# Kernel optimization log

Measured on AMD Instinct MI355X. Metric: run time of the kernel, lower is better.

Reference implementation:

```python
import jax, jax.numpy as jnp
import numpy as np

BN_EPS = 1e-5

def conv1x1(x, w, b):
    # x: [B,C,H,W], w: [O,C], b: [O]
    return jnp.einsum('bchw,oc->bohw', x, w) + b[None, :, None, None]

def maxpool2x2(x):
    B, C, H, W = x.shape
    return x.reshape(B, C, H // 2, 2, W // 2, 2).max(axis=(3, 5))

def setup_inputs() -> dict:
    key = jax.random.key(0)
    ks = jax.random.split(key, 11)
    B, C, H, W = 8, 256, 64, 64
    Ci = C // 2  # inter_channels = 128
    s_in = 1.0 / np.sqrt(C)
    s_int = 1.0 / np.sqrt(Ci)
    return {
        'x': jax.random.normal(ks[0], (B, C, H, W), jnp.float32),
        'theta_w': jax.random.uniform(ks[1], (Ci, C), jnp.float32, -s_in, s_in),
        'theta_b': jax.random.uniform(ks[2], (Ci,), jnp.float32, -s_in, s_in),
        'phi_w': jax.random.uniform(ks[3], (Ci, C), jnp.float32, -s_in, s_in),
        'phi_b': jax.random.uniform(ks[4], (Ci,), jnp.float32, -s_in, s_in),
        'g_w': jax.random.uniform(ks[5], (Ci, C), jnp.float32, -s_in, s_in),
        'g_b': jax.random.uniform(ks[6], (Ci,), jnp.float32, -s_in, s_in),
        'W_w': jax.random.uniform(ks[7], (C, Ci), jnp.float32, -s_int, s_int),
        'W_b': jax.random.uniform(ks[8], (C,), jnp.float32, -s_int, s_int),
        'bn_gamma': jax.random.normal(ks[9], (C,), jnp.float32) * 0.1 + 1.0,
        'bn_beta': jax.random.normal(ks[10], (C,), jnp.float32) * 0.1,
    }

def reference(x, theta_w, theta_b, phi_w, phi_b, g_w, g_b, W_w, W_b, bn_gamma, bn_beta):
    B, C, H, W = x.shape
    Ci = theta_w.shape[0]
    # g and phi are sub-sampled (2x2 maxpool) after the 1x1 conv
    g_x = maxpool2x2(conv1x1(x, g_w, g_b)).reshape(B, Ci, -1)        # [B,Ci,M]
    g_x = g_x.transpose(0, 2, 1)                                     # [B,M,Ci]
    theta_x = conv1x1(x, theta_w, theta_b).reshape(B, Ci, -1)        # [B,Ci,N]
    theta_x = theta_x.transpose(0, 2, 1)                             # [B,N,Ci]
    phi_x = maxpool2x2(conv1x1(x, phi_w, phi_b)).reshape(B, Ci, -1)  # [B,Ci,M]
    f = jnp.einsum('bnc,bcm->bnm', theta_x, phi_x)                   # [B,N,M]
    f_div_C = jax.nn.softmax(f, axis=-1)
    y = jnp.einsum('bnm,bmc->bnc', f_div_C, g_x)                     # [B,N,Ci]
    y = y.transpose(0, 2, 1).reshape(B, Ci, H, W)
    # 1x1 conv + BatchNorm2d (training-mode batch statistics)
    W_y = conv1x1(y, W_w, W_b)
    mean = W_y.mean(axis=(0, 2, 3))
    var = W_y.var(axis=(0, 2, 3))
    W_y = (W_y - mean[None, :, None, None]) * jax.lax.rsqrt(var + BN_EPS)[None, :, None, None]
    W_y = W_y * bn_gamma[None, :, None, None] + bn_beta[None, :, None, None]
    return W_y + x
```

## Files before the change

### kernel.cpp

```cpp
#include <hip/hip_runtime.h>
#include <hip/hip_bf16.h>
#include <cstdint>
#include <math.h>

using bf16 = __hip_bfloat16;
typedef __attribute__((ext_vector_type(8))) short bf16x8;
typedef __attribute__((ext_vector_type(4))) float f32x4;

#define DEV __device__ __forceinline__

DEV float b2f(unsigned short u) { return __uint_as_float(((uint32_t)u) << 16); }
DEV float bfl(bf16 h) { return __bfloat162float(h); }
DEV short f2bs(float f) { bf16 h = __float2bfloat16(f); return *(short*)&h; }
DEV uint32_t pk2(float a, float b) {
  return (uint32_t)(unsigned short)f2bs(a) |
         ((uint32_t)(unsigned short)f2bs(b) << 16);
}
DEV float ldv(const void* p, int isbf, int i) {
  return isbf ? bfl(((const bf16*)p)[i]) : ((const float*)p)[i];
}

DEV bf16x8 load_wfrag(const void* w, int isbf, int row, int K, int off) {
  bf16x8 r;
  if (isbf) {
    r = *(const bf16x8*)((const short*)w + (size_t)row * K + off);
  } else {
    const float* f = (const float*)w + (size_t)row * K + off;
    float4 a = *(const float4*)f, b = *(const float4*)(f + 4);
    r[0] = f2bs(a.x); r[1] = f2bs(a.y); r[2] = f2bs(a.z); r[3] = f2bs(a.w);
    r[4] = f2bs(b.x); r[5] = f2bs(b.y); r[6] = f2bs(b.z); r[7] = f2bs(b.w);
  }
  return r;
}

__global__ __launch_bounds__(256) void sniff_kernel(
    const unsigned short* __restrict__ xr, int* __restrict__ flag)
{
  int tid = threadIdx.x;
  int good = 0;
  for (int k = tid; k < 16384; k += 256) {
    unsigned short u = xr[2 * k];
    int e = (u >> 7) & 0xFF;
    good += (e >= 0x6A && e <= 0x86) ? 1 : 0;
  }
  __shared__ int r[256];
  r[tid] = good;
  __syncthreads();
  for (int off = 128; off; off >>= 1) {
    if (tid < off) r[tid] += r[tid + off];
    __syncthreads();
  }
  if (tid == 0) *flag = (r[0] > 9830) ? 1 : 0;
}

__global__ __launch_bounds__(256) void transpose_x(
    const void* __restrict__ x, short* __restrict__ xT, const int* __restrict__ flag)
{
  const int isbf = *flag;
  __shared__ short lt[64 * 71];
  const int n0 = blockIdx.x * 64, c0 = blockIdx.y * 64, b = blockIdx.z;
  const int tid = threadIdx.x;
  for (int it = 0; it < 4; ++it) {
    int idx4 = it * 256 + tid;
    int ci = idx4 >> 4, n4 = (idx4 & 15) * 4;
    size_t go = ((size_t)(b * 256 + c0 + ci)) * 4096 + n0 + n4;
    if (isbf) {
      ushort4 v = *(const ushort4*)((const unsigned short*)x + go);
      lt[ci * 71 + n4 + 0] = v.x; lt[ci * 71 + n4 + 1] = v.y;
      lt[ci * 71 + n4 + 2] = v.z; lt[ci * 71 + n4 + 3] = v.w;
    } else {
      float4 v = *(const float4*)((const float*)x + go);
      lt[ci * 71 + n4 + 0] = f2bs(v.x); lt[ci * 71 + n4 + 1] = f2bs(v.y);
      lt[ci * 71 + n4 + 2] = f2bs(v.z); lt[ci * 71 + n4 + 3] = f2bs(v.w);
    }
  }
  __syncthreads();
  for (int it = 0; it < 4; ++it) {
    int idx4 = it * 256 + tid;
    int n = idx4 >> 4, c4 = (idx4 & 15) * 4;
    ushort4 v;
    v.x = (unsigned short)lt[(c4 + 0) * 71 + n];
    v.y = (unsigned short)lt[(c4 + 1) * 71 + n];
    v.z = (unsigned short)lt[(c4 + 2) * 71 + n];
    v.w = (unsigned short)lt[(c4 + 3) * 71 + n];
    *(ushort4*)(xT + ((size_t)(b * 4096 + n0 + n)) * 256 + c0 + c4) = v;
  }
}

__global__ __launch_bounds__(256) void conv_tp_k(
    const short* __restrict__ xT,
    const void* __restrict__ w1, const void* __restrict__ b1, short* __restrict__ out1,
    const void* __restrict__ w2, const void* __restrict__ b2, short* __restrict__ out2,
    const int* __restrict__ flag)
{
  const int isbf = *flag;
  __shared__ short shA[64 * 264];
  __shared__ short shB[64 * 136];
  const int b = blockIdx.y, nbase = blockIdx.x * 64, tid = threadIdx.x;
  const int ln = tid & 15, q = (tid >> 4) & 3, wv = tid >> 6;
  for (int it = 0; it < 16; ++it) {
    int idx4 = it * 256 + tid;
    int n = idx4 >> 6, c4 = (idx4 & 63) * 4;
    *(ushort4*)&shA[n * 264 + c4] =
        *(const ushort4*)(xT + ((size_t)(b * 4096 + nbase + n)) * 256 + c4);
  }
  __syncthreads();
  f32x4 zero = {0.f, 0.f, 0.f, 0.f};
  f32x4 acc1[4][2], acc2[4][2];
  for (int nt = 0; nt < 4; ++nt)
    for (int ti = 0; ti < 2; ++ti) { acc1[nt][ti] = zero; acc2[nt][ti] = zero; }

  for (int kk = 0; kk < 8; ++kk) {
    int off = kk * 32 + q * 8;
    bf16x8 a[4];
    #pragma unroll
    for (int nt = 0; nt < 4; ++nt)
      a[nt] = *(const bf16x8*)&shA[(16 * nt + ln) * 264 + off];
    #pragma unroll
    for (int ti = 0; ti < 2; ++ti) {
      bf16x8 bw1 = load_wfrag(w1, isbf, 16 * (2 * wv + ti) + ln, 256, off);
      #pragma unroll
      for (int nt = 0; nt < 4; ++nt)
        acc1[nt][ti] = __builtin_amdgcn_mfma_f32_16x16x32_bf16(a[nt], bw1, acc1[nt][ti], 0, 0, 0);
    }
    #pragma unroll
    for (int ti = 0; ti < 2; ++ti) {
      bf16x8 bw2 = load_wfrag(w2, isbf, 16 * (2 * wv + ti) + ln, 256, off);
      #pragma unroll
      for (int nt = 0; nt < 4; ++nt)
        acc2[nt][ti] = __builtin_amdgcn_mfma_f32_16x16x32_bf16(a[nt], bw2, acc2[nt][ti], 0, 0, 0);
    }
  }
  {
    float bv[2];
    for (int ti = 0; ti < 2; ++ti) bv[ti] = ldv(b1, isbf, 16 * (2 * wv + ti) + ln);
    for (int nt = 0; nt < 4; ++nt)
      for (int ti = 0; ti < 2; ++ti)
        for (int r = 0; r < 4; ++r)
          shB[(16 * nt + q * 4 + r) * 136 + 16 * (2 * wv + ti) + ln] =
              f2bs(acc1[nt][ti][r] + bv[ti]);
    __syncthreads();
    for (int it = 0; it < 8; ++it) {
      int idx4 = it * 256 + tid;
      int n = idx4 >> 5, c4 = (idx4 & 31) * 4;
      *(ushort4*)(out1 + ((size_t)(b * 4096 + nbase + n)) * 128 + c4) =
          *(const ushort4*)&shB[n * 136 + c4];
    }
    __syncthreads();
  }
  {
    float bv[2];
    for (int ti = 0; ti < 2; ++ti) bv[ti] = ldv(b2, isbf, 16 * (2 * wv + ti) + ln);
    for (int nt = 0; nt < 4; ++nt)
      for (int ti = 0; ti < 2; ++ti)
        for (int r = 0; r < 4; ++r)
          shB[(16 * nt + q * 4 + r) * 136 + 16 * (2 * wv + ti) + ln] =
              f2bs(acc2[nt][ti][r] + bv[ti]);
    __syncthreads();
    for (int it = 0; it < 8; ++it) {
      int idx4 = it * 256 + tid;
      int n = idx4 >> 5, c4 = (idx4 & 31) * 4;
      *(ushort4*)(out2 + ((size_t)(b * 4096 + nbase + n)) * 128 + c4) =
          *(const ushort4*)&shB[n * 136 + c4];
    }
  }
}

__global__ __launch_bounds__(256) void conv_tpg_k(
    const short* __restrict__ xT,
    const void* __restrict__ w1, const void* __restrict__ b1, short* __restrict__ out1,
    const void* __restrict__ w2, const void* __restrict__ b2, short* __restrict__ out2,
    const void* __restrict__ w3, const void* __restrict__ b3, short* __restrict__ out3,
    const int* __restrict__ flag)
{
  const int isbf = *flag;
  __shared__ short shA[64 * 264];
  __shared__ short shB[8704];
  const int b = blockIdx.y, nbase = blockIdx.x * 64, tid = threadIdx.x;
  const int ln = tid & 15, q = (tid >> 4) & 3, wv = tid >> 6;
  for (int it = 0; it < 16; ++it) {
    int idx4 = it * 256 + tid;
    int n = idx4 >> 6, c4 = (idx4 & 63) * 4;
    *(ushort4*)&shA[n * 264 + c4] =
        *(const ushort4*)(xT + ((size_t)(b * 4096 + nbase + n)) * 256 + c4);
  }
  __syncthreads();
  f32x4 zero = {0.f, 0.f, 0.f, 0.f};
  f32x4 acc1[4][2], acc2[4][2], acc3[2][4];
  for (int nt = 0; nt < 4; ++nt)
    for (int ti = 0; ti < 2; ++ti) { acc1[nt][ti] = zero; acc2[nt][ti] = zero; }
  for (int ti = 0; ti < 2; ++ti)
    for (int nt = 0; nt < 4; ++nt) acc3[ti][nt] = zero;

  for (int kk = 0; kk < 8; ++kk) {
    int off = kk * 32 + q * 8;
    bf16x8 a[4];
    #pragma unroll
    for (int nt = 0; nt < 4; ++nt)
      a[nt] = *(const bf16x8*)&shA[(16 * nt + ln) * 264 + off];
    #pragma unroll
    for (int ti = 0; ti < 2; ++ti) {
      bf16x8 bw1 = load_wfrag(w1, isbf, 16 * (2 * wv + ti) + ln, 256, off);
      #pragma unroll
      for (int nt = 0; nt < 4; ++nt)
        acc1[nt][ti] = __builtin_amdgcn_mfma_f32_16x16x32_bf16(a[nt], bw1, acc1[nt][ti], 0, 0, 0);
    }
    #pragma unroll
    for (int ti = 0; ti < 2; ++ti) {
      bf16x8 bw2 = load_wfrag(w2, isbf, 16 * (2 * wv + ti) + ln, 256, off);
      #pragma unroll
      for (int nt = 0; nt < 4; ++nt)
        acc2[nt][ti] = __builtin_amdgcn_mfma_f32_16x16x32_bf16(a[nt], bw2, acc2[nt][ti], 0, 0, 0);
    }
    #pragma unroll
    for (int ti = 0; ti < 2; ++ti) {
      bf16x8 aw3 = load_wfrag(w3, isbf, 16 * (2 * wv + ti) + ln, 256, off);
      #pragma unroll
      for (int nt = 0; nt < 4; ++nt)
        acc3[ti][nt] = __builtin_amdgcn_mfma_f32_16x16x32_bf16(aw3, a[nt], acc3[ti][nt], 0, 0, 0);
    }
  }
  {
    float bv[2];
    for (int ti = 0; ti < 2; ++ti) bv[ti] = ldv(b1, isbf, 16 * (2 * wv + ti) + ln);
    for (int nt = 0; nt < 4; ++nt)
      for (int ti = 0; ti < 2; ++ti)
        for (int r = 0; r < 4; ++r)
          shB[(16 * nt + q * 4 + r) * 136 + 16 * (2 * wv + ti) + ln] =
              f2bs(acc1[nt][ti][r] + bv[ti]);
    __syncthreads();
    for (int it = 0; it < 8; ++it) {
      int idx4 = it * 256 + tid;
      int n = idx4 >> 5, c4 = (idx4 & 31) * 4;
      *(ushort4*)(out1 + ((size_t)(b * 4096 + nbase + n)) * 128 + c4) =
          *(const ushort4*)&shB[n * 136 + c4];
    }
    __syncthreads();
  }
  {
    float bv[2];
    for (int ti = 0; ti < 2; ++ti) bv[ti] = ldv(b2, isbf, 16 * (2 * wv + ti) + ln);
    for (int nt = 0; nt < 4; ++nt)
      for (int ti = 0; ti < 2; ++ti)
        for (int r = 0; r < 4; ++r)
          shB[(16 * nt + q * 4 + r) * 136 + 16 * (2 * wv + ti) + ln] =
              f2bs(acc2[nt][ti][r] + bv[ti]);
    __syncthreads();
    for (int it = 0; it < 8; ++it) {
      int idx4 = it * 256 + tid;
      int n = idx4 >> 5, c4 = (idx4 & 31) * 4;
      *(ushort4*)(out2 + ((size_t)(b * 4096 + nbase + n)) * 128 + c4) =
          *(const ushort4*)&shB[n * 136 + c4];
    }
    __syncthreads();
  }
  {
    for (int ti = 0; ti < 2; ++ti)
      for (int r = 0; r < 4; ++r) {
        int co = 16 * (2 * wv + ti) + q * 4 + r;
        float bb = ldv(b3, isbf, co);
        for (int nt = 0; nt < 4; ++nt)
          shB[co * 68 + 16 * nt + ln] = f2bs(acc3[ti][nt][r] + bb);
      }
    __syncthreads();
    for (int it = 0; it < 8; ++it) {
      int idx4 = it * 256 + tid;
      int co = idx4 >> 4, n4 = (idx4 & 15) * 4;
      *(ushort4*)(out3 + ((size_t)(b * 128 + co)) * 4096 + nbase + n4) =
          *(const ushort4*)&shB[co * 68 + n4];
    }
  }
}

template<int CO, int K>
__global__ __launch_bounds__(256) void conv_n_k(
    const short* __restrict__ inp, const void* __restrict__ w,
    const void* __restrict__ bias, short* __restrict__ out,
    const int* __restrict__ flag)
{
  const int isbf = *flag;
  constexpr int XS = 64 * (K + 8);
  constexpr int OS = CO * 68;
  __shared__ short sh[(XS > OS ? XS : OS)];
  const int b = blockIdx.y, nbase = blockIdx.x * 64, tid = threadIdx.x;
  const int ln = tid & 15, q = (tid >> 4) & 3, wv = tid >> 6;
  constexpr int TPW = CO / 64;
  constexpr int KS = (K == 256) ? 6 : 5;
  for (int it = 0; it < 64 * K / 1024; ++it) {
    int idx4 = it * 256 + tid;
    int n = idx4 >> KS, c4 = (idx4 & ((K / 4) - 1)) * 4;
    *(ushort4*)&sh[n * (K + 8) + c4] =
        *(const ushort4*)(inp + ((size_t)(b * 4096 + nbase + n)) * K + c4);
  }
  __syncthreads();
  f32x4 zero = {0.f, 0.f, 0.f, 0.f};
  f32x4 acc[TPW][4];
  for (int ti = 0; ti < TPW; ++ti) for (int nt = 0; nt < 4; ++nt) acc[ti][nt] = zero;

  for (int kk = 0; kk < K / 32; ++kk) {
    int off = kk * 32 + q * 8;
    bf16x8 bx[4];
    #pragma unroll
    for (int nt = 0; nt < 4; ++nt)
      bx[nt] = *(const bf16x8*)&sh[(16 * nt + ln) * (K + 8) + off];
    #pragma unroll
    for (int ti = 0; ti < TPW; ++ti) {
      bf16x8 aw = load_wfrag(w, isbf, 16 * (TPW * wv + ti) + ln, K, off);
      #pragma unroll
      for (int nt = 0; nt < 4; ++nt)
        acc[ti][nt] = __builtin_amdgcn_mfma_f32_16x16x32_bf16(aw, bx[nt], acc[ti][nt], 0, 0, 0);
    }
  }
  __syncthreads();
  for (int ti = 0; ti < TPW; ++ti)
    for (int r = 0; r < 4; ++r) {
      int co = 16 * (TPW * wv + ti) + q * 4 + r;
      float bb = ldv(bias, isbf, co);
      for (int nt = 0; nt < 4; ++nt)
        sh[co * 68 + 16 * nt + ln] = f2bs(acc[ti][nt][r] + bb);
    }
  __syncthreads();
  for (int it = 0; it < 64 * CO / 1024; ++it) {
    int idx4 = it * 256 + tid;
    int co = idx4 >> 4, n4 = (idx4 & 15) * 4;
    *(ushort4*)(out + ((size_t)(b * CO + co)) * 4096 + nbase + n4) =
        *(const ushort4*)&sh[co * 68 + n4];
  }
}

__global__ __launch_bounds__(256) void pool_phi_kernel(
    const short* __restrict__ pc, short* __restrict__ phi)
{
  int idx = blockIdx.x * 256 + threadIdx.x;
  int ci = idx & 127, m = (idx >> 7) & 1023, b = idx >> 17;
  int mh = m >> 5, mw = m & 31;
  const short* p = pc + ((size_t)(b * 4096 + (mh * 2) * 64 + mw * 2)) * 128 + ci;
  float v = fmaxf(fmaxf(b2f(p[0]), b2f(p[128])),
                  fmaxf(b2f(p[64 * 128]), b2f(p[65 * 128])));
  phi[idx] = f2bs(v);
}

__global__ __launch_bounds__(256) void pool_g_kernel(
    const short* __restrict__ gc, short* __restrict__ g)
{
  int idx = blockIdx.x * 256 + threadIdx.x;
  int m = idx & 1023, bc = idx >> 10;
  int mh = m >> 5, mw = m & 31;
  const short* p = gc + (size_t)bc * 4096 + mh * 128 + mw * 2;
  float v = fmaxf(fmaxf(b2f(p[0]), b2f(p[1])), fmaxf(b2f(p[64]), b2f(p[65])));
  g[idx] = f2bs(v);
}

__global__ __launch_bounds__(256) void pool_both_kernel(
    const short* __restrict__ pc, short* __restrict__ phi,
    const short* __restrict__ gc, short* __restrict__ g)
{
  int gidx = blockIdx.x * 256 + threadIdx.x;
  if (gidx < 1048576) {
    int idx = gidx;
    int ci = idx & 127, m = (idx >> 7) & 1023, b = idx >> 17;
    int mh = m >> 5, mw = m & 31;
    const short* p = pc + ((size_t)(b * 4096 + (mh * 2) * 64 + mw * 2)) * 128 + ci;
    float v = fmaxf(fmaxf(b2f(p[0]), b2f(p[128])),
                    fmaxf(b2f(p[64 * 128]), b2f(p[65 * 128])));
    phi[idx] = f2bs(v);
  } else {
    int idx = gidx - 1048576;
    int m = idx & 1023, bc = idx >> 10;
    int mh = m >> 5, mw = m & 31;
    const short* p = gc + (size_t)bc * 4096 + mh * 128 + mw * 2;
    float v = fmaxf(fmaxf(b2f(p[0]), b2f(p[1])), fmaxf(b2f(p[64]), b2f(p[65])));
    g[idx] = f2bs(v);
  }
}

__global__ __launch_bounds__(256) void attn_kernel(
    const short* __restrict__ theta, const short* __restrict__ phi,
    const short* __restrict__ g, short* __restrict__ y)
{
  __shared__ short ph[64 * 136];
  __shared__ short gl[128 * 72];
  __shared__ short Pl[64 * 72];
  const int b = blockIdx.y, nbase = blockIdx.x * 64, tid = threadIdx.x;
  const int ln = tid & 15, q = (tid >> 4) & 3, wv = tid >> 6;

  const int pm  = tid >> 5;
  const int pc4 = (tid & 31) * 4;
  const int gci = tid >> 4;
  const int gm4 = (tid & 15) * 4;
  const short* phb = phi + (size_t)b * 1024 * 128;
  const short* gb  = g   + (size_t)b * 128 * 1024;

  ushort4 pf_p[8], pf_g[8];
  #pragma unroll
  for (int it = 0; it < 8; ++it)
    pf_p[it] = *(const ushort4*)(phb + ((size_t)(pm + 8 * it)) * 128 + pc4);
  #pragma unroll
  for (int it = 0; it < 8; ++it)
    pf_g[it] = *(const ushort4*)(gb + ((size_t)(gci + 16 * it)) * 1024 + gm4);

  bf16x8 a[4];
  #pragma unroll
  for (int kk = 0; kk < 4; ++kk)
    a[kk] = *(const bf16x8*)(theta +
        ((size_t)(b * 4096 + nbase + 16 * wv + ln)) * 128 + kk * 32 + q * 8);

  f32x4 zero = {0.f, 0.f, 0.f, 0.f};
  f32x4 yacc[8], lacc = zero;
  #pragma unroll
  for (int t = 0; t < 8; ++t) yacc[t] = zero;
  bf16x8 ones;
  #pragma unroll
  for (int j = 0; j < 8; ++j) ones[j] = 0x3F80;

  for (int mc = 0; mc < 16; ++mc) {
    #pragma unroll
    for (int it = 0; it < 8; ++it)
      *(ushort4*)&ph[(pm + 8 * it) * 136 + pc4] = pf_p[it];
    #pragma unroll
    for (int it = 0; it < 8; ++it)
      *(ushort4*)&gl[(gci + 16 * it) * 72 + gm4] = pf_g[it];
    __syncthreads();

    if (mc < 15) {
      const int nmc = mc + 1;
      #pragma unroll
      for (int it = 0; it < 8; ++it)
        pf_p[it] = *(const ushort4*)(phb +
            ((size_t)(nmc * 64 + pm + 8 * it)) * 128 + pc4);
      #pragma unroll
      for (int it = 0; it < 8; ++it)
        pf_g[it] = *(const ushort4*)(gb +
            ((size_t)(gci + 16 * it)) * 1024 + nmc * 64 + gm4);
    }

    #pragma unroll
    for (int t = 0; t < 4; ++t) {
      f32x4 s = zero;
      #pragma unroll
      for (int kk = 0; kk < 4; ++kk) {
        bf16x8 bp = *(const bf16x8*)&ph[(16 * t + ln) * 136 + kk * 32 + q * 8];
        s = __builtin_amdgcn_mfma_f32_16x16x32_bf16(a[kk], bp, s, 0, 0, 0);
      }
      #pragma unroll
      for (int r = 0; r < 4; ++r)
        Pl[(16 * wv + q * 4 + r) * 72 + 16 * t + ln] =
            f2bs(__expf(fminf(s[r], 80.f)));
    }
    bf16x8 ap[2];
    #pragma unroll
    for (int kk = 0; kk < 2; ++kk)
      ap[kk] = *(const bf16x8*)&Pl[(16 * wv + ln) * 72 + kk * 32 + q * 8];
    #pragma unroll
    for (int kk = 0; kk < 2; ++kk)
      lacc = __builtin_amdgcn_mfma_f32_16x16x32_bf16(ap[kk], ones, lacc, 0, 0, 0);
    #pragma unroll
    for (int t = 0; t < 8; ++t) {
      #pragma unroll
      for (int kk = 0; kk < 2; ++kk) {
        bf16x8 bg = *(const bf16x8*)&gl[(16 * t + ln) * 72 + kk * 32 + q * 8];
        yacc[t] = __builtin_amdgcn_mfma_f32_16x16x32_bf16(ap[kk], bg, yacc[t], 0, 0, 0);
      }
    }
    __syncthreads();
  }

  float li[4];
  #pragma unroll
  for (int r = 0; r < 4; ++r) li[r] = 1.0f / lacc[r];
  for (int t = 0; t < 8; ++t)
    for (int r = 0; r < 4; ++r)
      ph[(16 * wv + q * 4 + r) * 136 + 16 * t + ln] = f2bs(yacc[t][r] * li[r]);
  __syncthreads();
  for (int it = 0; it < 8; ++it) {
    int idx4 = it * 256 + tid;
    int n = idx4 >> 5, c4 = (idx4 & 31) * 4;
    *(ushort4*)(y + ((size_t)(b * 4096 + nbase + n)) * 128 + c4) =
        *(const ushort4*)&ph[n * 136 + c4];
  }
}

__global__ __launch_bounds__(256, 4) void convW_k(
    const short* __restrict__ yb, const void* __restrict__ w,
    const void* __restrict__ bias, short* __restrict__ Wy,
    float* __restrict__ stats, const int* __restrict__ flag)
{
  const int isbf = *flag;
  __shared__ short sh[256 * 72];
  const int b = blockIdx.y, nbase = blockIdx.x * 64, tid = threadIdx.x;
  const int ln = tid & 15, q = (tid >> 4) & 3, wv = tid >> 6;

  for (int it = 0; it < 4; ++it) {
    int idx8 = it * 256 + tid;
    int n = idx8 >> 4, c8 = (idx8 & 15) * 8;
    *(uint4*)&sh[n * 136 + c8] =
        *(const uint4*)(yb + ((size_t)(b * 4096 + nbase + n)) * 128 + c8);
  }
  __syncthreads();
  f32x4 zero = {0.f, 0.f, 0.f, 0.f};
  f32x4 acc[4][4];
  for (int ti = 0; ti < 4; ++ti)
    for (int nt = 0; nt < 4; ++nt) acc[ti][nt] = zero;

  for (int kk = 0; kk < 4; ++kk) {
    int off = kk * 32 + q * 8;
    bf16x8 bx[4];
    #pragma unroll
    for (int nt = 0; nt < 4; ++nt)
      bx[nt] = *(const bf16x8*)&sh[(16 * nt + ln) * 136 + off];
    #pragma unroll
    for (int ti = 0; ti < 4; ++ti) {
      bf16x8 aw = load_wfrag(w, isbf, 16 * (4 * wv + ti) + ln, 128, off);
      #pragma unroll
      for (int nt = 0; nt < 4; ++nt)
        acc[ti][nt] = __builtin_amdgcn_mfma_f32_16x16x32_bf16(aw, bx[nt], acc[ti][nt], 0, 0, 0);
    }
  }
  __syncthreads();
  #pragma unroll
  for (int ti = 0; ti < 4; ++ti)
    #pragma unroll
    for (int r = 0; r < 4; ++r) {
      int co = 16 * (4 * wv + ti) + 4 * q + r;
      float bb = ldv(bias, isbf, co);
      #pragma unroll
      for (int nt = 0; nt < 4; ++nt)
        sh[co * 72 + 16 * nt + ln] = f2bs(acc[ti][nt][r] + bb);
    }
  __syncthreads();
  {
    int co = tid;
    float s = 0.f, s2 = 0.f;
    for (int i = 0; i < 64; ++i) {
      float v = b2f((unsigned short)sh[co * 72 + i]);
      s += v; s2 += v * v;
    }
    atomicAdd(&stats[co], s);
    atomicAdd(&stats[256 + co], s2);
  }
  for (int it = 0; it < 8; ++it) {
    int idx8 = it * 256 + tid;
    int co = idx8 >> 3, n8 = (idx8 & 7) * 8;
    *(uint4*)(Wy + ((size_t)(b * 256 + co)) * 4096 + nbase + n8) =
        *(const uint4*)&sh[co * 72 + n8];
  }
}

__global__ __launch_bounds__(256) void bn_apply4(
    const short* __restrict__ Wy, const void* __restrict__ x,
    const float* __restrict__ stats, const void* __restrict__ gamma,
    const void* __restrict__ beta, void* __restrict__ out,
    const int* __restrict__ flag)
{
  const int isbf = *flag;
  int t = blockIdx.x * 256 + threadIdx.x;
  int idx4 = t * 4;
  int c = (idx4 >> 12) & 255;
  float s = stats[c], s2 = stats[256 + c];
  float mean = s * (1.0f / 32768.0f);
  float var = fmaxf(s2 * (1.0f / 32768.0f) - mean * mean, 0.f);
  float scale = rsqrtf(var + 1e-5f) * ldv(gamma, isbf, c);
  float shift = ldv(beta, isbf, c) - mean * scale;
  ushort4 wy = *(const ushort4*)(Wy + idx4);
  float xv[4];
  if (isbf) {
    ushort4 xu = *(const ushort4*)((const unsigned short*)x + idx4);
    xv[0] = b2f(xu.x); xv[1] = b2f(xu.y); xv[2] = b2f(xu.z); xv[3] = b2f(xu.w);
  } else {
    float4 xf = *(const float4*)((const float*)x + idx4);
    xv[0] = xf.x; xv[1] = xf.y; xv[2] = xf.z; xv[3] = xf.w;
  }
  float v0 = b2f(wy.x) * scale + shift + xv[0];
  float v1 = b2f(wy.y) * scale + shift + xv[1];
  float v2 = b2f(wy.z) * scale + shift + xv[2];
  float v3 = b2f(wy.w) * scale + shift + xv[3];
  if (isbf) {
    uint2 o; o.x = pk2(v0, v1); o.y = pk2(v2, v3);
    *(uint2*)((unsigned short*)out + idx4) = o;
  } else {
    float4 o = make_float4(v0, v1, v2, v3);
    *(float4*)((float*)out + idx4) = o;
  }
}

extern "C" void kernel_launch(void* const* d_in, const int* in_sizes, int n_in,
                              void* d_out, int out_size, void* d_ws, size_t ws_size,
                              hipStream_t stream) {
  const void* x       = d_in[0];
  const void* theta_w = d_in[1];
  const void* theta_b = d_in[2];
  const void* phi_w   = d_in[3];
  const void* phi_b   = d_in[4];
  const void* g_w     = d_in[5];
  const void* g_b     = d_in[6];
  const void* W_w     = d_in[7];
  const void* W_b     = d_in[8];
  const void* gamma   = d_in[9];
  const void* beta    = d_in[10];

  char* wsb = (char*)d_ws;
  short* xT      = (short*)(wsb + 0);
  short* ybuf    = (short*)(wsb + 0);
  short* theta   = (short*)(wsb + 16777216);
  short* W_y     = (short*)(wsb + 16777216);
  short* scratch = (short*)(wsb + 25165824);
  short* phi     = (short*)(wsb + 33554432);
  short* gg      = (short*)(wsb + 35651584);
  float* stats   = (float*)(wsb + 37748736);
  int*   flag    = (int*)  (wsb + 37750784);
  short* g_c     = (short*)(wsb + 37752832);
  const bool fused = ws_size >= (size_t)37752832 + 8388608;

  dim3 blk(256);
  dim3 cgrid(64, 8);
  dim3 tgrid(64, 4, 8);

  hipMemsetAsync(stats, 0, 2048, stream);
  sniff_kernel<<<1, blk, 0, stream>>>((const unsigned short*)x, flag);
  transpose_x<<<tgrid, blk, 0, stream>>>(x, xT, flag);
  if (fused) {
    conv_tpg_k<<<cgrid, blk, 0, stream>>>(xT, theta_w, theta_b, theta,
                                          phi_w, phi_b, scratch,
                                          g_w, g_b, g_c, flag);
    pool_both_kernel<<<8192, blk, 0, stream>>>(scratch, phi, g_c, gg);
  } else {
    conv_tp_k<<<cgrid, blk, 0, stream>>>(xT, theta_w, theta_b, theta,
                                         phi_w, phi_b, scratch, flag);
    pool_phi_kernel<<<4096, blk, 0, stream>>>(scratch, phi);
    conv_n_k<128, 256><<<cgrid, blk, 0, stream>>>(xT, g_w, g_b, scratch, flag);
    pool_g_kernel<<<4096, blk, 0, stream>>>(scratch, gg);
  }
  attn_kernel<<<cgrid, blk, 0, stream>>>(theta, phi, gg, ybuf);
  convW_k<<<cgrid, blk, 0, stream>>>(ybuf, W_w, W_b, W_y, stats, flag);
  bn_apply4<<<8192, blk, 0, stream>>>(W_y, x, stats, gamma, beta, d_out, flag);
}
```

Baseline: 231.3 us.

## Fuse attention output with W 1x1 conv and BN stats kernel

Merges the attention kernel and the W-projection conv kernel. The normalized attention output tile stays in shared memory and feeds the W conv MFMAs directly, so the y buffer is never written to or read back from global memory and one launch is removed. Shared memory is reused through a union between the gl/Pl attention buffers and the conv output staging. The fused kernel has higher register and LDS pressure, which may lower occupancy. It also drops the launch bound of 4 blocks per SM that convW_k used.

```diff
diff --git a/kernel.cpp b/kernel.cpp
--- a/kernel.cpp
+++ b/kernel.cpp
@@ -374,13 +374,20 @@
   }
 }
 
-__global__ __launch_bounds__(256) void attn_kernel(
+__global__ __launch_bounds__(256) void attn_convW_k(
     const short* __restrict__ theta, const short* __restrict__ phi,
-    const short* __restrict__ g, short* __restrict__ y)
+    const short* __restrict__ g,
+    const void* __restrict__ w, const void* __restrict__ bias,
+    short* __restrict__ Wy, float* __restrict__ stats,
+    const int* __restrict__ flag)
 {
   __shared__ short ph[64 * 136];
-  __shared__ short gl[128 * 72];
-  __shared__ short Pl[64 * 72];
+  __shared__ __align__(16) char rest[36864];
+  short* gl = (short*)rest;
+  short* Pl = (short*)(rest + 18432);
+  short* shW = (short*)rest;
+
+  const int isbf = *flag;
   const int b = blockIdx.y, nbase = blockIdx.x * 64, tid = threadIdx.x;
   const int ln = tid & 15, q = (tid >> 4) & 3, wv = tid >> 6;
 
@@ -472,32 +479,7 @@
     for (int r = 0; r < 4; ++r)
       ph[(16 * wv + q * 4 + r) * 136 + 16 * t + ln] = f2bs(yacc[t][r] * li[r]);
   __syncthreads();
-  for (int it = 0; it < 8; ++it) {
-    int idx4 = it * 256 + tid;
-    int n = idx4 >> 5, c4 = (idx4 & 31) * 4;
-    *(ushort4*)(y + ((size_t)(b * 4096 + nbase + n)) * 128 + c4) =
-        *(const ushort4*)&ph[n * 136 + c4];
-  }
-}
-
-__global__ __launch_bounds__(256, 4) void convW_k(
-    const short* __restrict__ yb, const void* __restrict__ w,
-    const void* __restrict__ bias, short* __restrict__ Wy,
-    float* __restrict__ stats, const int* __restrict__ flag)
-{
-  const int isbf = *flag;
-  __shared__ short sh[256 * 72];
-  const int b = blockIdx.y, nbase = blockIdx.x * 64, tid = threadIdx.x;
-  const int ln = tid & 15, q = (tid >> 4) & 3, wv = tid >> 6;
-
-  for (int it = 0; it < 4; ++it) {
-    int idx8 = it * 256 + tid;
-    int n = idx8 >> 4, c8 = (idx8 & 15) * 8;
-    *(uint4*)&sh[n * 136 + c8] =
-        *(const uint4*)(yb + ((size_t)(b * 4096 + nbase + n)) * 128 + c8);
-  }
-  __syncthreads();
-  f32x4 zero = {0.f, 0.f, 0.f, 0.f};
+
   f32x4 acc[4][4];
   for (int ti = 0; ti < 4; ++ti)
     for (int nt = 0; nt < 4; ++nt) acc[ti][nt] = zero;
@@ -507,7 +489,7 @@
     bf16x8 bx[4];
     #pragma unroll
     for (int nt = 0; nt < 4; ++nt)
-      bx[nt] = *(const bf16x8*)&sh[(16 * nt + ln) * 136 + off];
+      bx[nt] = *(const bf16x8*)&ph[(16 * nt + ln) * 136 + off];
     #pragma unroll
     for (int ti = 0; ti < 4; ++ti) {
       bf16x8 aw = load_wfrag(w, isbf, 16 * (4 * wv + ti) + ln, 128, off);
@@ -516,7 +498,6 @@
         acc[ti][nt] = __builtin_amdgcn_mfma_f32_16x16x32_bf16(aw, bx[nt], acc[ti][nt], 0, 0, 0);
     }
   }
-  __syncthreads();
   #pragma unroll
   for (int ti = 0; ti < 4; ++ti)
     #pragma unroll
@@ -525,14 +506,14 @@
       float bb = ldv(bias, isbf, co);
       #pragma unroll
       for (int nt = 0; nt < 4; ++nt)
-        sh[co * 72 + 16 * nt + ln] = f2bs(acc[ti][nt][r] + bb);
+        shW[co * 72 + 16 * nt + ln] = f2bs(acc[ti][nt][r] + bb);
     }
   __syncthreads();
   {
     int co = tid;
     float s = 0.f, s2 = 0.f;
     for (int i = 0; i < 64; ++i) {
-      float v = b2f((unsigned short)sh[co * 72 + i]);
+      float v = b2f((unsigned short)shW[co * 72 + i]);
       s += v; s2 += v * v;
     }
     atomicAdd(&stats[co], s);
@@ -542,7 +523,7 @@
     int idx8 = it * 256 + tid;
     int co = idx8 >> 3, n8 = (idx8 & 7) * 8;
     *(uint4*)(Wy + ((size_t)(b * 256 + co)) * 4096 + nbase + n8) =
-        *(const uint4*)&sh[co * 72 + n8];
+        *(const uint4*)&shW[co * 72 + n8];
   }
 }
 
@@ -600,9 +581,8 @@
 
   char* wsb = (char*)d_ws;
   short* xT      = (short*)(wsb + 0);
-  short* ybuf    = (short*)(wsb + 0);
+  short* Wy      = (short*)(wsb + 0);
   short* theta   = (short*)(wsb + 16777216);
-  short* W_y     = (short*)(wsb + 16777216);
   short* scratch = (short*)(wsb + 25165824);
   short* phi     = (short*)(wsb + 33554432);
   short* gg      = (short*)(wsb + 35651584);
@@ -630,7 +610,7 @@
     conv_n_k<128, 256><<<cgrid, blk, 0, stream>>>(xT, g_w, g_b, scratch, flag);
     pool_g_kernel<<<4096, blk, 0, stream>>>(scratch, gg);
   }
-  attn_kernel<<<cgrid, blk, 0, stream>>>(theta, phi, gg, ybuf);
-  convW_k<<<cgrid, blk, 0, stream>>>(ybuf, W_w, W_b, W_y, stats, flag);
-  bn_apply4<<<8192, blk, 0, stream>>>(W_y, x, stats, gamma, beta, d_out, flag);
-}
+  attn_convW_k<<<cgrid, blk, 0, stream>>>(theta, phi, gg,
+                                          W_w, W_b, Wy, stats, flag);
+  bn_apply4<<<8192, blk, 0, stream>>>(Wy, x, stats, gamma, beta, d_out, flag);
+}
```

Result: faster. 221.4 us (-4.3%).
